# Kernel tuning notes

Hardware: AMD Instinct MI355X
Metric: run time of the kernel (lower is better)

The kernel has to match this reference:

```python
import jax, jax.numpy as jnp
import numpy as np

T, B = 21, 4096
H, E, V = 1024, 50, 96
PAD = 0


def setup_inputs() -> dict:
    key = jax.random.key(0)
    ks = jax.random.split(key, 10)
    s_e = 1.0 / np.sqrt(H)  # torch LSTM init scale
    emb = jax.random.normal(ks[0], (V, E), jnp.float32)
    emb = emb.at[PAD].set(0.0)  # padding_idx row is zero
    return {
        "input_ids": jax.random.randint(ks[1], (T, B), 0, V),
        "h0": jax.random.normal(ks[2], (1, B, H), jnp.float32),
        "c0": jax.random.normal(ks[3], (1, B, H), jnp.float32),
        "emb": emb,
        "W_ih": jax.random.uniform(ks[4], (4 * H, E), jnp.float32, -s_e, s_e),
        "W_hh": jax.random.uniform(ks[5], (4 * H, H), jnp.float32, -s_e, s_e),
        "b_ih": jax.random.uniform(ks[6], (4 * H,), jnp.float32, -s_e, s_e),
        "b_hh": jax.random.uniform(ks[7], (4 * H,), jnp.float32, -s_e, s_e),
        "W_out": jax.random.uniform(ks[8], (V, H), jnp.float32, -s_e, s_e),
        "b_out": jax.random.uniform(ks[9], (V,), jnp.float32, -s_e, s_e),
    }


def reference(input_ids, h0, c0, emb, W_ih, W_hh, b_ih, b_hh, W_out, b_out):
    # char_embeds: (T, B, E)
    x = emb[input_ids]
    # Precompute input projections for all timesteps in one GEMM: (T, B, 4H)
    x_proj = jnp.einsum("tbe,ge->tbg", x, W_ih) + b_ih + b_hh

    def step(carry, xp_t):
        h, c = carry  # (B, H) each
        gates = xp_t + h @ W_hh.T  # (B, 4H), torch gate order i,f,g,o
        i, f, g, o = jnp.split(gates, 4, axis=-1)
        i = jax.nn.sigmoid(i)
        f = jax.nn.sigmoid(f)
        g = jnp.tanh(g)
        o = jax.nn.sigmoid(o)
        c = f * c + i * g
        h = o * jnp.tanh(c)
        return (h, c), h

    (h_T, c_T), h_ts = jax.lax.scan(step, (h0[0], c0[0]), x_proj)
    # char_output_projection: (T, B, V)
    scores = jnp.einsum("tbh,vh->tbv", h_ts, W_out) + b_out
    return scores, (h_T[None], c_T[None])
```

## Files before the change

kernel.cpp:

```cpp
#include <hip/hip_runtime.h>
#include <hip/hip_bf16.h>


#define T_STEPS 21
#define BSZ 4096
#define HDIM 1024
#define VOCAB 96
#define EDIM 50

typedef __attribute__((ext_vector_type(8))) short short8;
typedef __attribute__((ext_vector_type(4))) float f32x4;

#define GLL16(g, l)                                                        \
  __builtin_amdgcn_global_load_lds(                                        \
      (const __attribute__((address_space(1))) void*)(g),                  \
      (__attribute__((address_space(3))) void*)(l), 16, 0, 0)

__device__ __forceinline__ float sigmoidf_fast(float x) {
  return 1.0f / (1.0f + __expf(-x));
}
__device__ __forceinline__ float tanhf_fast(float x) {
  return 2.0f / (1.0f + __expf(-2.0f * x)) - 1.0f;
}

__global__ void prep_convert(const float* __restrict__ Whh_f,
                             const float* __restrict__ Wout_f,
                             const float* __restrict__ h0,
                             __hip_bfloat16* __restrict__ Whh,
                             __hip_bfloat16* __restrict__ Wout,
                             __hip_bfloat16* __restrict__ hb0) {
  int idx = blockIdx.x * 256 + threadIdx.x;
  if (idx < 4 * HDIM * HDIM) {
    Whh[idx] = __float2bfloat16(Whh_f[idx]);
    hb0[idx] = __float2bfloat16(h0[idx]);
  }
  if (idx < VOCAB * HDIM) Wout[idx] = __float2bfloat16(Wout_f[idx]);
}

__global__ void prep_ptable(const float* __restrict__ emb,
                            const float* __restrict__ Wih,
                            const float* __restrict__ bih,
                            const float* __restrict__ bhh,
                            float* __restrict__ P) {
  int idx = blockIdx.x * 256 + threadIdx.x;
  int v = idx >> 12, g = idx & 4095;
  const float* er = emb + v * EDIM;
  const float* wr = Wih + g * EDIM;
  float s = bih[g] + bhh[g];
#pragma unroll 10
  for (int e = 0; e < EDIM; ++e) s += er[e] * wr[e];
  P[idx] = s;
}

template <bool LAST>
__global__ __launch_bounds__(256, 2) void lstm_step_kernel(
    const int* __restrict__ ids,
    const __hip_bfloat16* __restrict__ hprev,
    const __hip_bfloat16* __restrict__ Whh,
    const float* __restrict__ P,
    const float* __restrict__ c_in,
    float* __restrict__ c_out,
    __hip_bfloat16* __restrict__ hnext,
    float* __restrict__ hf32)
{
  __shared__ __align__(16) __hip_bfloat16 sA[128 * 64];
  __shared__ __align__(16) __hip_bfloat16 sB[128 * 64];

  const int tid = threadIdx.x;
  const int wave = tid >> 6;
  const int lane = tid & 63;
  const int m0 = blockIdx.x * 128;
  const int j0 = blockIdx.y * 32;

  f32x4 acc[4][4] = {};

  const int lrow = lane >> 3;
  const int lcol = (lane & 7) * 8;

  int brow_g[4];
#pragma unroll
  for (int i = 0; i < 4; ++i) {
    int n = wave * 32 + i * 8 + lrow;
    int q = n >> 6, gate = (n >> 4) & 3, u = n & 15;
    brow_g[i] = gate * HDIM + j0 + q * 16 + u;
  }
  const __hip_bfloat16* Abase = hprev + (size_t)(m0 + wave * 32 + lrow) * HDIM + lcol;

  const int mw = (wave >> 1) * 64;
  const int nw = (wave & 1) * 64;
  const int u16 = lane & 15;
  const int k8 = (lane >> 4) * 8;

  for (int k0 = 0; k0 < HDIM; k0 += 64) {
#pragma unroll
    for (int i = 0; i < 4; ++i) {
      GLL16(Abase + i * 8 * HDIM + k0, &sA[(wave * 32 + i * 8) * 64]);
      GLL16(Whh + (size_t)brow_g[i] * HDIM + k0 + lcol, &sB[(wave * 32 + i * 8) * 64]);
    }
    __syncthreads();
#pragma unroll
    for (int kk = 0; kk < 64; kk += 32) {
      short8 af[4], bf[4];
#pragma unroll
      for (int mi = 0; mi < 4; ++mi)
        af[mi] = *(const short8*)&sA[(mw + mi * 16 + u16) * 64 + kk + k8];
#pragma unroll
      for (int ni = 0; ni < 4; ++ni)
        bf[ni] = *(const short8*)&sB[(nw + ni * 16 + u16) * 64 + kk + k8];
#pragma unroll
      for (int mi = 0; mi < 4; ++mi)
#pragma unroll
        for (int ni = 0; ni < 4; ++ni)
          acc[mi][ni] = __builtin_amdgcn_mfma_f32_16x16x32_bf16(
              af[mi], bf[ni], acc[mi][ni], 0, 0, 0);
    }
    __syncthreads();
  }

  const int q = wave & 1;
  const int j = j0 + q * 16 + u16;
  const int rb = m0 + mw + (lane >> 4) * 4;
#pragma unroll
  for (int mi = 0; mi < 4; ++mi) {
#pragma unroll
    for (int r = 0; r < 4; ++r) {
      int row = rb + mi * 16 + r;
      int id = ids[row];
      const float* Pr = P + id * 4096 + j;
      float iv = acc[mi][0][r] + Pr[0];
      float fv = acc[mi][1][r] + Pr[1024];
      float gv = acc[mi][2][r] + Pr[2048];
      float ov = acc[mi][3][r] + Pr[3072];
      iv = sigmoidf_fast(iv);
      fv = sigmoidf_fast(fv);
      gv = tanhf_fast(gv);
      ov = sigmoidf_fast(ov);
      size_t off = (size_t)row * HDIM + j;
      float cc = fv * c_in[off] + iv * gv;
      c_out[off] = cc;
      float hh = ov * tanhf_fast(cc);
      hnext[off] = __float2bfloat16(hh);
      if (LAST) hf32[off] = hh;
    }
  }
}

__global__ __launch_bounds__(256, 2) void scores_kernel(
    const __hip_bfloat16* __restrict__ h,
    const __hip_bfloat16* __restrict__ Wout,
    const float* __restrict__ bout,
    float* __restrict__ out)
{
  const int tid = threadIdx.x;
  const int wave = tid >> 6, lane = tid & 63;
  const int u = lane & 15, k8 = (lane >> 4) * 8;
  const long r0 = (long)blockIdx.x * 64 + wave * 16;
  f32x4 acc[6] = {};
  const __hip_bfloat16* hr = h + (r0 + u) * HDIM + k8;
  for (int k0 = 0; k0 < HDIM; k0 += 32) {
    short8 a = *(const short8*)(hr + k0);
#pragma unroll
    for (int ni = 0; ni < 6; ++ni) {
      short8 b = *(const short8*)(Wout + (ni * 16 + u) * HDIM + k0 + k8);
      acc[ni] = __builtin_amdgcn_mfma_f32_16x16x32_bf16(a, b, acc[ni], 0, 0, 0);
    }
  }
  const long rowb = r0 + (lane >> 4) * 4;
#pragma unroll
  for (int ni = 0; ni < 6; ++ni) {
    int v = ni * 16 + u;
    float bv = bout[v];
#pragma unroll
    for (int r = 0; r < 4; ++r) out[(rowb + r) * VOCAB + v] = acc[ni][r] + bv;
  }
}

extern "C" void kernel_launch(void* const* d_in, const int* in_sizes, int n_in,
                              void* d_out, int out_size, void* d_ws, size_t ws_size,
                              hipStream_t stream) {
  const int* ids = (const int*)d_in[0];
  const float* h0 = (const float*)d_in[1];
  const float* c0 = (const float*)d_in[2];
  const float* emb = (const float*)d_in[3];
  const float* Wih = (const float*)d_in[4];
  const float* Whh_f = (const float*)d_in[5];
  const float* bih = (const float*)d_in[6];
  const float* bhh = (const float*)d_in[7];
  const float* Wout_f = (const float*)d_in[8];
  const float* bout = (const float*)d_in[9];

  float* out = (float*)d_out;
  float* scores = out;
  float* hT = out + (size_t)T_STEPS * BSZ * VOCAB;
  float* cT = hT + (size_t)BSZ * HDIM;

  const size_t BH = (size_t)BSZ * HDIM;
  char* w = (char*)d_ws;
  float* P = (float*)w;              w += (size_t)VOCAB * 4096 * 4;
  __hip_bfloat16* Whh = (__hip_bfloat16*)w;  w += (size_t)4 * HDIM * HDIM * 2;
  __hip_bfloat16* Wout = (__hip_bfloat16*)w; w += (size_t)VOCAB * HDIM * 2;
  __hip_bfloat16* hts = (__hip_bfloat16*)w;
  size_t base = (size_t)VOCAB * 4096 * 4 + (size_t)4 * HDIM * HDIM * 2 +
                (size_t)VOCAB * HDIM * 2;
  const bool full = ws_size >= base + (size_t)(T_STEPS + 1) * BH * 2;

  prep_convert<<<dim3((4 * HDIM * HDIM + 255) / 256), dim3(256), 0, stream>>>(
      Whh_f, Wout_f, h0, Whh, Wout, hts);
  prep_ptable<<<dim3((VOCAB * 4096) / 256), dim3(256), 0, stream>>>(
      emb, Wih, bih, bhh, P);

  for (int t = 0; t < T_STEPS; ++t) {
    __hip_bfloat16* hp = hts + (full ? (size_t)t * BH : (size_t)(t & 1) * BH);
    __hip_bfloat16* hn = hts + (full ? (size_t)(t + 1) * BH : (size_t)((t + 1) & 1) * BH);
    const float* cin = (t == 0) ? c0 : cT;
    if (t == T_STEPS - 1) {
      lstm_step_kernel<true><<<dim3(32, 32), dim3(256), 0, stream>>>(
          ids + (size_t)t * BSZ, hp, Whh, P, cin, cT, hn, hT);
    } else {
      lstm_step_kernel<false><<<dim3(32, 32), dim3(256), 0, stream>>>(
          ids + (size_t)t * BSZ, hp, Whh, P, cin, cT, hn, nullptr);
    }
    if (!full) {
      scores_kernel<<<dim3(BSZ / 64), dim3(256), 0, stream>>>(
          hn, Wout, bout, scores + (size_t)t * BSZ * VOCAB);
    }
  }
  if (full) {
    scores_kernel<<<dim3(T_STEPS * BSZ / 64), dim3(256), 0, stream>>>(
        hts + BH, Wout, bout, scores);
  }
}
```

Measured before the change: 1.290 ms.

## Swizzle LDS tiles, stage P slice in LDS, tile scores GEMM through LDS

The LSTM step kernel now XOR-swizzles the 16-byte chunk positions of its LDS tiles to avoid bank conflicts on MFMA fragment reads. After the GEMM it also stages this block's 32-column slice of the input-projection table (all 96 vocab rows × 4 gates) into reused LDS, so the epilogue reads P from LDS rather than doing gathered global loads. The scores kernel is rewritten to stage h and W_out tiles in swizzled LDS with 128-row blocks, replacing direct global fragment loads. The cost is extra LDS footprint (48KB in the step kernel), which may limit occupancy, plus an added sync and P load per block.

```diff
diff --git a/kernel.cpp b/kernel.cpp
--- a/kernel.cpp
+++ b/kernel.cpp
@@ -63,8 +63,10 @@
     __hip_bfloat16* __restrict__ hnext,
     float* __restrict__ hf32)
 {
-  __shared__ __align__(16) __hip_bfloat16 sA[128 * 64];
-  __shared__ __align__(16) __hip_bfloat16 sB[128 * 64];
+  __shared__ __align__(16) char smem[49152];
+  __hip_bfloat16* sA = (__hip_bfloat16*)smem;
+  __hip_bfloat16* sB = (__hip_bfloat16*)(smem + 16384);
+  float* sP = (float*)smem;
 
   const int tid = threadIdx.x;
   const int wave = tid >> 6;
@@ -75,7 +77,7 @@
   f32x4 acc[4][4] = {};
 
   const int lrow = lane >> 3;
-  const int lcol = (lane & 7) * 8;
+  const int lcol = ((lane & 7) ^ lrow) * 8;
 
   int brow_g[4];
 #pragma unroll
@@ -84,29 +86,32 @@
     int q = n >> 6, gate = (n >> 4) & 3, u = n & 15;
     brow_g[i] = gate * HDIM + j0 + q * 16 + u;
   }
-  const __hip_bfloat16* Abase = hprev + (size_t)(m0 + wave * 32 + lrow) * HDIM + lcol;
+  const __hip_bfloat16* Abase =
+      hprev + (size_t)(m0 + wave * 32 + lrow) * HDIM + lcol;
 
   const int mw = (wave >> 1) * 64;
   const int nw = (wave & 1) * 64;
   const int u16 = lane & 15;
-  const int k8 = (lane >> 4) * 8;
+  const int k16q = lane >> 4;
 
   for (int k0 = 0; k0 < HDIM; k0 += 64) {
 #pragma unroll
     for (int i = 0; i < 4; ++i) {
       GLL16(Abase + i * 8 * HDIM + k0, &sA[(wave * 32 + i * 8) * 64]);
-      GLL16(Whh + (size_t)brow_g[i] * HDIM + k0 + lcol, &sB[(wave * 32 + i * 8) * 64]);
+      GLL16(Whh + (size_t)brow_g[i] * HDIM + k0 + lcol,
+            &sB[(wave * 32 + i * 8) * 64]);
     }
     __syncthreads();
 #pragma unroll
     for (int kk = 0; kk < 64; kk += 32) {
+      const int sl = (((kk >> 3) + k16q) ^ (u16 & 7)) * 8;
       short8 af[4], bf[4];
 #pragma unroll
       for (int mi = 0; mi < 4; ++mi)
-        af[mi] = *(const short8*)&sA[(mw + mi * 16 + u16) * 64 + kk + k8];
+        af[mi] = *(const short8*)&sA[(mw + mi * 16 + u16) * 64 + sl];
 #pragma unroll
       for (int ni = 0; ni < 4; ++ni)
-        bf[ni] = *(const short8*)&sB[(nw + ni * 16 + u16) * 64 + kk + k8];
+        bf[ni] = *(const short8*)&sB[(nw + ni * 16 + u16) * 64 + sl];
 #pragma unroll
       for (int mi = 0; mi < 4; ++mi)
 #pragma unroll
@@ -117,20 +122,33 @@
     __syncthreads();
   }
 
+  {
+    const int pchunk = lane & 7;
+#pragma unroll
+    for (int i = 0; i < 12; ++i) {
+      int p = wave * 96 + i * 8 + (lane >> 3);
+      int v = p >> 2, gate = p & 3;
+      GLL16(P + (size_t)v * 4096 + gate * 1024 + j0 + pchunk * 4,
+            &sP[(wave * 96 + i * 8) * 32]);
+    }
+  }
+  __syncthreads();
+
   const int q = wave & 1;
-  const int j = j0 + q * 16 + u16;
-  const int rb = m0 + mw + (lane >> 4) * 4;
+  const int jo = q * 16 + u16;
+  const int j = j0 + jo;
+  const int rb = m0 + mw + k16q * 4;
 #pragma unroll
   for (int mi = 0; mi < 4; ++mi) {
 #pragma unroll
     for (int r = 0; r < 4; ++r) {
       int row = rb + mi * 16 + r;
       int id = ids[row];
-      const float* Pr = P + id * 4096 + j;
+      const float* Pr = &sP[id * 128 + jo];
       float iv = acc[mi][0][r] + Pr[0];
-      float fv = acc[mi][1][r] + Pr[1024];
-      float gv = acc[mi][2][r] + Pr[2048];
-      float ov = acc[mi][3][r] + Pr[3072];
+      float fv = acc[mi][1][r] + Pr[32];
+      float gv = acc[mi][2][r] + Pr[64];
+      float ov = acc[mi][3][r] + Pr[96];
       iv = sigmoidf_fast(iv);
       fv = sigmoidf_fast(fv);
       gv = tanhf_fast(gv);
@@ -151,27 +169,65 @@
     const float* __restrict__ bout,
     float* __restrict__ out)
 {
+  __shared__ __align__(16) __hip_bfloat16 sA[128 * 128];
+  __shared__ __align__(16) __hip_bfloat16 sB[96 * 128];
+
   const int tid = threadIdx.x;
   const int wave = tid >> 6, lane = tid & 63;
-  const int u = lane & 15, k8 = (lane >> 4) * 8;
-  const long r0 = (long)blockIdx.x * 64 + wave * 16;
-  f32x4 acc[6] = {};
-  const __hip_bfloat16* hr = h + (r0 + u) * HDIM + k8;
-  for (int k0 = 0; k0 < HDIM; k0 += 32) {
-    short8 a = *(const short8*)(hr + k0);
-#pragma unroll
-    for (int ni = 0; ni < 6; ++ni) {
-      short8 b = *(const short8*)(Wout + (ni * 16 + u) * HDIM + k0 + k8);
-      acc[ni] = __builtin_amdgcn_mfma_f32_16x16x32_bf16(a, b, acc[ni], 0, 0, 0);
-    }
-  }
-  const long rowb = r0 + (lane >> 4) * 4;
+  const int u16 = lane & 15, k16q = lane >> 4;
+  const long r0 = (long)blockIdx.x * 128;
+
+  f32x4 acc[2][6] = {};
+
+  const int srow4 = lane >> 4;
+  const int sslot = lane & 15;
+
+  for (int k0 = 0; k0 < HDIM; k0 += 128) {
+#pragma unroll
+    for (int i = 0; i < 8; ++i) {
+      int row = wave * 32 + i * 4 + srow4;
+      int g = sslot ^ (row & 15);
+      GLL16(h + (r0 + row) * HDIM + k0 + g * 8, &sA[(wave * 32 + i * 4) * 128]);
+    }
+#pragma unroll
+    for (int i = 0; i < 6; ++i) {
+      int row = wave * 24 + i * 4 + srow4;
+      int g = sslot ^ (row & 15);
+      GLL16(Wout + (size_t)row * HDIM + k0 + g * 8,
+            &sB[(wave * 24 + i * 4) * 128]);
+    }
+    __syncthreads();
+#pragma unroll
+    for (int kk = 0; kk < 128; kk += 32) {
+      const int sl = (((kk >> 3) + k16q) ^ u16) * 8;
+      short8 af[2], bf[6];
+#pragma unroll
+      for (int mi = 0; mi < 2; ++mi)
+        af[mi] = *(const short8*)&sA[(wave * 32 + mi * 16 + u16) * 128 + sl];
+#pragma unroll
+      for (int ni = 0; ni < 6; ++ni)
+        bf[ni] = *(const short8*)&sB[(ni * 16 + u16) * 128 + sl];
+#pragma unroll
+      for (int mi = 0; mi < 2; ++mi)
+#pragma unroll
+        for (int ni = 0; ni < 6; ++ni)
+          acc[mi][ni] = __builtin_amdgcn_mfma_f32_16x16x32_bf16(
+              af[mi], bf[ni], acc[mi][ni], 0, 0, 0);
+    }
+    __syncthreads();
+  }
+
 #pragma unroll
   for (int ni = 0; ni < 6; ++ni) {
-    int v = ni * 16 + u;
+    int v = ni * 16 + u16;
     float bv = bout[v];
 #pragma unroll
-    for (int r = 0; r < 4; ++r) out[(rowb + r) * VOCAB + v] = acc[ni][r] + bv;
+    for (int mi = 0; mi < 2; ++mi)
+#pragma unroll
+      for (int r = 0; r < 4; ++r) {
+        long grow = r0 + wave * 32 + mi * 16 + k16q * 4 + r;
+        out[grow * VOCAB + v] = acc[mi][ni][r] + bv;
+      }
   }
 }
 
@@ -221,12 +277,12 @@
           ids + (size_t)t * BSZ, hp, Whh, P, cin, cT, hn, nullptr);
     }
     if (!full) {
-      scores_kernel<<<dim3(BSZ / 64), dim3(256), 0, stream>>>(
+      scores_kernel<<<dim3(BSZ / 128), dim3(256), 0, stream>>>(
           hn, Wout, bout, scores + (size_t)t * BSZ * VOCAB);
     }
   }
   if (full) {
-    scores_kernel<<<dim3(T_STEPS * BSZ / 64), dim3(256), 0, stream>>>(
+    scores_kernel<<<dim3(T_STEPS * BSZ / 128), dim3(256), 0, stream>>>(
         hts + BH, Wout, bout, scores);
   }
 }
```

Result: faster. 1.208 ms (-6.4%).
